# Kernel optimization log

Measured on AMD Instinct MI355X. Metric: run time of the kernel, lower is better.

The kernel has to match this reference:

```python
import jax, jax.numpy as jnp
import numpy as np

N = 50000   # nodes
E = 500000  # edges (before self-loops)
H = 4       # heads
C = 128     # per-head channels
DIN = 182
D1 = H * C  # 512
LN_EPS = 1e-5
NEG_SLOPE = 0.2


def setup_inputs():
    key = jax.random.key(0)
    ks = jax.random.split(key, 26)
    def rn(k, shape, s=0.05):
        return jax.random.normal(k, shape, jnp.float32) * s
    return {
        'x': jax.random.normal(ks[0], (N, DIN), jnp.float32),
        'edge_index': jax.random.randint(ks[1], (2, E), 0, N, jnp.int32),
        # GAT layer 1 (182 -> 4x128)
        'W1': rn(ks[2], (DIN, D1)), 'as1': rn(ks[3], (H, C)), 'ad1': rn(ks[4], (H, C)), 'b1': rn(ks[5], (D1,)),
        # LayerNorm 1
        'g1': jnp.ones((D1,), jnp.float32), 'bn1': jnp.zeros((D1,), jnp.float32),
        # Expansion MLP 512->512->256
        'We1': rn(ks[6], (D1, D1)), 'bE1': rn(ks[7], (D1,)),
        'We2': rn(ks[8], (D1, 256)), 'bE2': rn(ks[9], (256,)),
        # Residual projection 512->256 + learned scale
        'Wr': rn(ks[10], (D1, 256)), 'br': rn(ks[11], (256,)),
        'rscale': jnp.float32(0.5),
        # GAT layer 2 (256 -> 4x128)
        'W2': rn(ks[12], (256, D1)), 'as2': rn(ks[13], (H, C)), 'ad2': rn(ks[14], (H, C)), 'b2': rn(ks[15], (D1,)),
        # LayerNorm 2
        'g2': jnp.ones((D1,), jnp.float32), 'bn2': jnp.zeros((D1,), jnp.float32),
        # Classifier 512->512->2
        'Wc1': rn(ks[16], (D1, D1)), 'bc1': rn(ks[17], (D1,)),
        'Wc2': rn(ks[18], (D1, 2)), 'bc2': rn(ks[19], (2,)),
    }


def layer_norm(x, g, b):
    mu = jnp.mean(x, axis=-1, keepdims=True)
    var = jnp.mean(jnp.square(x - mu), axis=-1, keepdims=True)
    return (x - mu) * jax.lax.rsqrt(var + LN_EPS) * g + b


def gat_conv(x, src, dst, W, a_src, a_dst, bias):
    # PyG GATConv (eval mode, self-loops already in src/dst), concat heads.
    h = (x @ W).reshape(N, H, C)                     # [N,H,C]
    al_s = jnp.sum(h * a_src, axis=-1)               # [N,H]
    al_d = jnp.sum(h * a_dst, axis=-1)               # [N,H]
    e = jax.nn.leaky_relu(al_s[src] + al_d[dst], NEG_SLOPE)  # [E',H]
    m = jax.ops.segment_max(e, dst, num_segments=N)  # segment softmax over target nbhd
    ex = jnp.exp(e - m[dst])
    denom = jax.ops.segment_sum(ex, dst, num_segments=N)
    alpha = ex / denom[dst]                          # [E',H]
    msg = h[src] * alpha[:, :, None]                 # [E',H,C]
    out = jax.ops.segment_sum(msg, dst, num_segments=N)
    return out.reshape(N, H * C) + bias


def reference(x, edge_index, W1, as1, ad1, b1, g1, bn1, We1, bE1, We2, bE2,
              Wr, br, rscale, W2, as2, ad2, b2, g2, bn2, Wc1, bc1, Wc2, bc2):
    loops = jnp.arange(N, dtype=edge_index.dtype)
    src = jnp.concatenate([edge_index[0], loops])    # add self-loops (PyG default)
    dst = jnp.concatenate([edge_index[1], loops])

    h1 = gat_conv(x, src, dst, W1, as1, ad1, b1)
    h1 = jax.nn.elu(layer_norm(h1, g1, bn1))
    h_exp = jax.nn.relu(h1 @ We1 + bE1) @ We2 + bE2  # expansion MLP (dropout=eval)
    h_comb = (h1 @ Wr + br) + rscale * h_exp         # residual combine

    h2 = gat_conv(h_comb, src, dst, W2, as2, ad2, b2)
    h2 = jax.nn.elu(layer_norm(h2, g2, bn2))
    out = jax.nn.relu(h2 @ Wc1 + bc1) @ Wc2 + bc2    # classifier -> [N,2]
    return out
```

## Files before the change

### kernel.cpp

```cpp
#include <hip/hip_runtime.h>
#include <hip/hip_bf16.h>
#include <math.h>

#define NNODES 50000
#define NEDGES 500000
#define NTOT   (NEDGES + NNODES)
#define MPAD   50048
#define D1     512
#define NH     4
#define LN_EPS 1e-5f
#define NEG_SLOPE 0.2f

#define SBLK 256
#define NSB  ((NNODES + SBLK - 1) / SBLK)

typedef __attribute__((ext_vector_type(8))) short short8;
typedef __attribute__((ext_vector_type(4))) float f32x4;
typedef __hip_bfloat16 bf16;

#define GLDS16(g, l) __builtin_amdgcn_global_load_lds( \
    (const __attribute__((address_space(1))) void*)(g), \
    (__attribute__((address_space(3))) void*)(l), 16, 0, 0)

__device__ __forceinline__ float bf2f(short u) {
    unsigned int x = ((unsigned int)(unsigned short)u) << 16;
    return __uint_as_float(x);
}
__device__ __forceinline__ short f2bf(float f) {
    unsigned int x = __float_as_uint(f);
    unsigned int r = (x + 0x7fffu + ((x >> 16) & 1u)) >> 16;
    return (short)r;
}
__device__ __forceinline__ float leaky(float e) {
    return (e >= 0.f) ? e : NEG_SLOPE * e;
}


__global__ void k_count(const int* __restrict__ ei, int* __restrict__ counts) {
    int e = blockIdx.x * blockDim.x + threadIdx.x;
    if (e >= NTOT) return;
    int d = (e < NEDGES) ? ei[NEDGES + e] : (e - NEDGES);
    atomicAdd(&counts[d], 1);
}

__global__ void k_scan1(const int* __restrict__ counts, int* __restrict__ offs,
                        int* __restrict__ bsums) {
    __shared__ int s[SBLK];
    int tid = threadIdx.x, b = blockIdx.x;
    int idx = b * SBLK + tid;
    int v = (idx < NNODES) ? counts[idx] : 0;
    s[tid] = v;
    __syncthreads();
    for (int d = 1; d < SBLK; d <<= 1) {
        int t = (tid >= d) ? s[tid - d] : 0;
        __syncthreads();
        s[tid] += t;
        __syncthreads();
    }
    if (idx < NNODES) offs[idx] = s[tid] - v;
    if (tid == SBLK - 1) bsums[b] = s[tid];
}

__global__ void k_scan2(const int* __restrict__ bsums, int* __restrict__ bbase) {
    __shared__ int s[256];
    int tid = threadIdx.x;
    int v = (tid < NSB) ? bsums[tid] : 0;
    s[tid] = v;
    __syncthreads();
    for (int d = 1; d < 256; d <<= 1) {
        int t = (tid >= d) ? s[tid - d] : 0;
        __syncthreads();
        s[tid] += t;
        __syncthreads();
    }
    bbase[tid] = s[tid] - v;
    if (tid == 255) bbase[256] = s[255];
}

__global__ void k_scan3(int* __restrict__ offs, const int* __restrict__ bbase,
                        int* __restrict__ cursor) {
    int idx = blockIdx.x * 256 + threadIdx.x;
    if (idx < NNODES) {
        int v = offs[idx] + bbase[idx >> 8];
        offs[idx] = v;
        cursor[idx] = v;
    }
    if (idx == 0) offs[NNODES] = bbase[256];
}

__global__ void k_fill(const int* __restrict__ ei, int* __restrict__ cursor,
                       int* __restrict__ srcs) {
    int e = blockIdx.x * blockDim.x + threadIdx.x;
    if (e >= NTOT) return;
    int s, d;
    if (e < NEDGES) { s = ei[e]; d = ei[NEDGES + e]; }
    else            { s = d = e - NEDGES; }
    int pos = atomicAdd(&cursor[d], 1);
    srcs[pos] = s;
}


__global__ void k_wt_all(const float* __restrict__ W1, const float* __restrict__ We1,
                         const float* __restrict__ We2, const float* __restrict__ Wr,
                         const float* __restrict__ W2, const float* __restrict__ Wc1,
                         bf16* __restrict__ W1t, bf16* __restrict__ We1t,
                         bf16* __restrict__ We2t, bf16* __restrict__ Wrt,
                         bf16* __restrict__ W2t, bf16* __restrict__ Wc1t) {
    int which = blockIdx.y;
    const float* W; bf16* Wt; int K, N, Kpad;
    switch (which) {
        case 0:  W = W1;  Wt = W1t;  K = 182; N = 512; Kpad = 192; break;
        case 1:  W = We1; Wt = We1t; K = 512; N = 512; Kpad = 512; break;
        case 2:  W = We2; Wt = We2t; K = 512; N = 256; Kpad = 512; break;
        case 3:  W = Wr;  Wt = Wrt;  K = 512; N = 256; Kpad = 512; break;
        case 4:  W = W2;  Wt = W2t;  K = 256; N = 512; Kpad = 256; break;
        default: W = Wc1; Wt = Wc1t; K = 512; N = 512; Kpad = 512; break;
    }
    int idx = blockIdx.x * 256 + threadIdx.x;
    if (idx >= N * Kpad) return;
    int n = idx / Kpad, k = idx % Kpad;
    float v = (k < K) ? W[(size_t)k * N + n] : 0.f;
    Wt[idx] = __float2bfloat16(v);
}

__global__ void k_xconv(const float* __restrict__ x, bf16* __restrict__ xb) {
    int idx = blockIdx.x * 256 + threadIdx.x;
    if (idx >= MPAD * 192) return;
    int r = idx / 192, k = idx % 192;
    float v = (r < NNODES && k < 182) ? x[(size_t)r * 182 + k] : 0.f;
    xb[idx] = __float2bfloat16(v);
}


__global__ __launch_bounds__(256) void k_edge_alpha(
        const float* __restrict__ als, const float* __restrict__ ald,
        const int* __restrict__ offs, const int* __restrict__ srcs,
        float* __restrict__ alpha) {
    int tid = threadIdx.x;
    int n = blockIdx.x * 4 + (tid >> 6);
    if (n >= NNODES) return;
    int lane = tid & 63;
    int head = lane >> 4, sub = lane & 15;
    int e0 = offs[n], e1 = offs[n + 1];
    float adh = ald[n * NH + head];

    float m = -1e30f;
    for (int k = e0 + sub; k < e1; k += 16)
        m = fmaxf(m, leaky(als[srcs[k] * NH + head] + adh));
    #pragma unroll
    for (int o = 1; o < 16; o <<= 1) m = fmaxf(m, __shfl_xor(m, o));
    float d = 0.f;
    for (int k = e0 + sub; k < e1; k += 16)
        d += __expf(leaky(als[srcs[k] * NH + head] + adh) - m);
    #pragma unroll
    for (int o = 1; o < 16; o <<= 1) d += __shfl_xor(d, o);
    float dinv = 1.f / d;
    for (int k = e0 + sub; k < e1; k += 16)
        alpha[k * NH + head] = __expf(leaky(als[srcs[k] * NH + head] + adh) - m) * dinv;
}


__global__ __launch_bounds__(256) void k_gat_aggregate(
        const bf16* __restrict__ h, const float* __restrict__ alpha,
        const int* __restrict__ offs, const int* __restrict__ srcs,
        const float* __restrict__ bias, const float* __restrict__ gamma,
        const float* __restrict__ beta, bf16* __restrict__ out) {
    int tid = threadIdx.x;
    int n = blockIdx.x * 4 + (tid >> 6);
    if (n >= NNODES) return;
    int lane = tid & 63;
    int head = lane >> 4;
    int ch0 = lane * 8;
    int e0 = offs[n], e1 = offs[n + 1];

    float acc[8] = {};
    for (int base = e0; base < e1; base += 64) {
        int cnt = min(64, e1 - base);
        int sv = (base + lane < e1) ? srcs[base + lane] : 0;
        int k = 0;
        for (; k + 4 <= cnt; k += 4) {
            int s0 = __shfl(sv, k),     s1 = __shfl(sv, k + 1);
            int s2 = __shfl(sv, k + 2), s3 = __shfl(sv, k + 3);
            float p0 = alpha[(base + k)     * NH + head];
            float p1 = alpha[(base + k + 1) * NH + head];
            float p2 = alpha[(base + k + 2) * NH + head];
            float p3 = alpha[(base + k + 3) * NH + head];
            short8 h0 = *reinterpret_cast<const short8*>(&h[(size_t)s0 * D1 + ch0]);
            short8 h1 = *reinterpret_cast<const short8*>(&h[(size_t)s1 * D1 + ch0]);
            short8 h2 = *reinterpret_cast<const short8*>(&h[(size_t)s2 * D1 + ch0]);
            short8 h3 = *reinterpret_cast<const short8*>(&h[(size_t)s3 * D1 + ch0]);
            #pragma unroll
            for (int j = 0; j < 8; j++)
                acc[j] += p0 * bf2f(h0[j]) + p1 * bf2f(h1[j])
                        + p2 * bf2f(h2[j]) + p3 * bf2f(h3[j]);
        }
        for (; k < cnt; k++) {
            int s0 = __shfl(sv, k);
            float p0 = alpha[(base + k) * NH + head];
            short8 h0 = *reinterpret_cast<const short8*>(&h[(size_t)s0 * D1 + ch0]);
            #pragma unroll
            for (int j = 0; j < 8; j++) acc[j] += p0 * bf2f(h0[j]);
        }
    }

    float v[8];
    float ps = 0.f;
    #pragma unroll
    for (int j = 0; j < 8; j++) { v[j] = acc[j] + bias[ch0 + j]; ps += v[j]; }
    #pragma unroll
    for (int o = 1; o < 64; o <<= 1) ps += __shfl_xor(ps, o);
    float mu = ps * (1.f / 512.f);
    float qs = 0.f;
    #pragma unroll
    for (int j = 0; j < 8; j++) { float dvj = v[j] - mu; qs += dvj * dvj; }
    #pragma unroll
    for (int o = 1; o < 64; o <<= 1) qs += __shfl_xor(qs, o);
    float rstd = rsqrtf(qs * (1.f / 512.f) + LN_EPS);

    short8 ov;
    #pragma unroll
    for (int j = 0; j < 8; j++) {
        float y = (v[j] - mu) * rstd * gamma[ch0 + j] + beta[ch0 + j];
        float e = (y > 0.f) ? y : (__expf(y) - 1.f);
        ov[j] = f2bf(e);
    }
    *reinterpret_cast<short8*>(&out[(size_t)n * D1 + ch0]) = ov;
}


#define EPI_BF_LOG   0
#define EPI_BRELU_BF 1
#define EPI_CLS      2

template<int EPI>
__global__ __launch_bounds__(256) void gemm64(
    const ushort* __restrict__ A, const ushort* __restrict__ Bt,
    const float* __restrict__ bias, bf16* __restrict__ Obf,
    float* __restrict__ Of32, const float* __restrict__ Wc2,
    int Mreal, int N, int K, const float* __restrict__ bc2,
    const float* __restrict__ a_s, const float* __restrict__ a_d,
    float* __restrict__ als, float* __restrict__ ald) {
    __shared__ __align__(16) ushort As[128 * 64];
    __shared__ __align__(16) ushort Bs[128 * 64];
    int tid = threadIdx.x;
    int wave = tid >> 6, lane = tid & 63;
    int brow = blockIdx.x * 128;
    int bcol = blockIdx.y * 128;
    int wm = (wave >> 1) * 64, wn = (wave & 1) * 64;
    int lr = lane & 15, hi = lane >> 4;
    int rx = lr & 7;
    int r8 = lane >> 3;
    int slotsw = (lane & 7) ^ r8;

    f32x4 acc[4][4] = {};

    for (int k0 = 0; k0 < K; k0 += 64) {
        if (k0) __syncthreads();
        #pragma unroll
        for (int i = 0; i < 4; i++) {
            int rb = wave * 32 + i * 8;
            GLDS16(A  + (size_t)(brow + rb + r8) * K + k0 + slotsw * 8, As + rb * 64);
            GLDS16(Bt + (size_t)(bcol + rb + r8) * K + k0 + slotsw * 8, Bs + rb * 64);
        }
        __syncthreads();

        #pragma unroll
        for (int sub = 0; sub < 2; sub++) {
            short8 af[4], bfr[4];
            int bsl = ((sub * 4 + hi) ^ rx) * 8;
            #pragma unroll
            for (int f = 0; f < 4; f++) {
                af[f]  = *reinterpret_cast<const short8*>(&As[(wm + f * 16 + lr) * 64 + bsl]);
                bfr[f] = *reinterpret_cast<const short8*>(&Bs[(wn + f * 16 + lr) * 64 + bsl]);
            }
            #pragma unroll
            for (int fm = 0; fm < 4; fm++)
                #pragma unroll
                for (int fn = 0; fn < 4; fn++)
                    acc[fm][fn] = __builtin_amdgcn_mfma_f32_16x16x32_bf16(
                        af[fm], bfr[fn], acc[fm][fn], 0, 0, 0);
        }
    }

    if (EPI == EPI_BF_LOG) {
        int head = bcol >> 7;
        float asr[4], adr[4];
        #pragma unroll
        for (int fn = 0; fn < 4; fn++) {
            int col = bcol + wn + fn * 16 + lr;
            asr[fn] = a_s[col]; adr[fn] = a_d[col];
        }
        #pragma unroll
        for (int fm = 0; fm < 4; fm++) {
            int row0 = brow + wm + fm * 16 + hi * 4;
            #pragma unroll
            for (int r = 0; r < 4; r++) {
                int row = row0 + r;
                bool ok = row < Mreal;
                float s1 = 0.f, s2 = 0.f;
                #pragma unroll
                for (int fn = 0; fn < 4; fn++) {
                    float v = acc[fm][fn][r];
                    if (ok) Obf[(size_t)row * N + bcol + wn + fn * 16 + lr] = __float2bfloat16(v);
                    s1 += v * asr[fn];
                    s2 += v * adr[fn];
                }
                #pragma unroll
                for (int o = 1; o < 16; o <<= 1) {
                    s1 += __shfl_xor(s1, o);
                    s2 += __shfl_xor(s2, o);
                }
                if (ok && lr == 0) {
                    atomicAdd(&als[row * NH + head], s1);
                    atomicAdd(&ald[row * NH + head], s2);
                }
            }
        }
        return;
    }

    if (EPI == EPI_CLS) {
        float w2[4][2], b4[4];
        #pragma unroll
        for (int fn = 0; fn < 4; fn++) {
            int col = bcol + wn + fn * 16 + lr;
            w2[fn][0] = Wc2[col * 2];
            w2[fn][1] = Wc2[col * 2 + 1];
            b4[fn] = bias[col];
        }
        #pragma unroll
        for (int fm = 0; fm < 4; fm++) {
            #pragma unroll
            for (int r = 0; r < 4; r++) {
                int row = brow + wm + fm * 16 + hi * 4 + r;
                float s0 = 0.f, s1 = 0.f;
                #pragma unroll
                for (int fn = 0; fn < 4; fn++) {
                    float v = acc[fm][fn][r] + b4[fn];
                    v = v > 0.f ? v : 0.f;
                    s0 += v * w2[fn][0];
                    s1 += v * w2[fn][1];
                }
                #pragma unroll
                for (int o = 1; o < 16; o <<= 1) {
                    s0 += __shfl_xor(s0, o);
                    s1 += __shfl_xor(s1, o);
                }
                if (lr == 0 && row < Mreal) {
                    if (bcol == 0 && wn == 0) { s0 += bc2[0]; s1 += bc2[1]; }
                    atomicAdd(&Of32[row * 2],     s0);
                    atomicAdd(&Of32[row * 2 + 1], s1);
                }
            }
        }
        return;
    }

    #pragma unroll
    for (int fm = 0; fm < 4; fm++) {
        int row0 = brow + wm + fm * 16 + hi * 4;
        #pragma unroll
        for (int fn = 0; fn < 4; fn++) {
            int col = bcol + wn + fn * 16 + lr;
            #pragma unroll
            for (int r = 0; r < 4; r++) {
                int row = row0 + r;
                if (row >= Mreal) continue;
                float v = acc[fm][fn][r] + bias[col];
                v = v > 0.f ? v : 0.f;
                Obf[(size_t)row * N + col] = __float2bfloat16(v);
            }
        }
    }
}


__global__ __launch_bounds__(256) void gemm_dual64(
    const ushort* __restrict__ A1, const ushort* __restrict__ B1t,
    const ushort* __restrict__ A2, const ushort* __restrict__ B2t,
    const float* __restrict__ bias1, const float* __restrict__ bias2,
    bf16* __restrict__ Obf, int Mreal, int N, int K,
    const float* __restrict__ rsc) {
    __shared__ __align__(16) ushort As[128 * 64];
    __shared__ __align__(16) ushort Bs[128 * 64];
    int tid = threadIdx.x;
    int wave = tid >> 6, lane = tid & 63;
    int brow = blockIdx.x * 128;
    int bcol = blockIdx.y * 128;
    int wm = (wave >> 1) * 64, wn = (wave & 1) * 64;
    int lr = lane & 15, hi = lane >> 4;
    int rx = lr & 7;
    int r8 = lane >> 3;
    int slotsw = (lane & 7) ^ r8;
    float rs = *rsc;

    f32x4 acc[4][4] = {};

    #pragma unroll
    for (int phase = 0; phase < 2; phase++) {
        const ushort* Ap = phase ? A2 : A1;
        const ushort* Bp = phase ? B2t : B1t;
        if (phase) {
            __syncthreads();
            #pragma unroll
            for (int fm = 0; fm < 4; fm++)
                #pragma unroll
                for (int fn = 0; fn < 4; fn++)
                    #pragma unroll
                    for (int r = 0; r < 4; r++) acc[fm][fn][r] *= rs;
        }
        for (int k0 = 0; k0 < K; k0 += 64) {
            if (k0 || phase) __syncthreads();
            #pragma unroll
            for (int i = 0; i < 4; i++) {
                int rb = wave * 32 + i * 8;
                GLDS16(Ap + (size_t)(brow + rb + r8) * K + k0 + slotsw * 8, As + rb * 64);
                GLDS16(Bp + (size_t)(bcol + rb + r8) * K + k0 + slotsw * 8, Bs + rb * 64);
            }
            __syncthreads();

            #pragma unroll
            for (int sub = 0; sub < 2; sub++) {
                short8 af[4], bfr[4];
                int bsl = ((sub * 4 + hi) ^ rx) * 8;
                #pragma unroll
                for (int f = 0; f < 4; f++) {
                    af[f]  = *reinterpret_cast<const short8*>(&As[(wm + f * 16 + lr) * 64 + bsl]);
                    bfr[f] = *reinterpret_cast<const short8*>(&Bs[(wn + f * 16 + lr) * 64 + bsl]);
                }
                #pragma unroll
                for (int fm = 0; fm < 4; fm++)
                    #pragma unroll
                    for (int fn = 0; fn < 4; fn++)
                        acc[fm][fn] = __builtin_amdgcn_mfma_f32_16x16x32_bf16(
                            af[fm], bfr[fn], acc[fm][fn], 0, 0, 0);
            }
        }
    }

    #pragma unroll
    for (int fm = 0; fm < 4; fm++) {
        int row0 = brow + wm + fm * 16 + hi * 4;
        #pragma unroll
        for (int fn = 0; fn < 4; fn++) {
            int col = bcol + wn + fn * 16 + lr;
            float be = bias2[col] + rs * bias1[col];
            #pragma unroll
            for (int r = 0; r < 4; r++) {
                int row = row0 + r;
                if (row >= Mreal) continue;
                Obf[(size_t)row * N + col] = __float2bfloat16(acc[fm][fn][r] + be);
            }
        }
    }
}


extern "C" void kernel_launch(void* const* d_in, const int* in_sizes, int n_in,
                              void* d_out, int out_size, void* d_ws, size_t ws_size,
                              hipStream_t stream) {
    const float* x   = (const float*)d_in[0];
    const int*   ei  = (const int*)d_in[1];
    const float* W1  = (const float*)d_in[2];
    const float* as1 = (const float*)d_in[3];
    const float* ad1 = (const float*)d_in[4];
    const float* b1  = (const float*)d_in[5];
    const float* g1  = (const float*)d_in[6];
    const float* bn1 = (const float*)d_in[7];
    const float* We1 = (const float*)d_in[8];
    const float* bE1 = (const float*)d_in[9];
    const float* We2 = (const float*)d_in[10];
    const float* bE2 = (const float*)d_in[11];
    const float* Wr  = (const float*)d_in[12];
    const float* br  = (const float*)d_in[13];
    const float* rsc = (const float*)d_in[14];
    const float* W2  = (const float*)d_in[15];
    const float* as2 = (const float*)d_in[16];
    const float* ad2 = (const float*)d_in[17];
    const float* b2  = (const float*)d_in[18];
    const float* g2  = (const float*)d_in[19];
    const float* bn2 = (const float*)d_in[20];
    const float* Wc1 = (const float*)d_in[21];
    const float* bc1 = (const float*)d_in[22];
    const float* Wc2 = (const float*)d_in[23];
    const float* bc2 = (const float*)d_in[24];
    float* out = (float*)d_out;

    char* ws = (char*)d_ws;
    size_t o = 0;
    auto alloc = [&](size_t bytes) { void* p = ws + o; o += (bytes + 255) & ~255ull; return p; };
    bf16* xb    = (bf16*)alloc((size_t)MPAD * 192 * 2);
    bf16* bufA  = (bf16*)alloc((size_t)MPAD * D1 * 2);
    bf16* bufB  = (bf16*)alloc((size_t)MPAD * D1 * 2);
    bf16* bufC  = (bf16*)alloc((size_t)MPAD * D1 * 2);
    bf16* hcb   = (bf16*)alloc((size_t)MPAD * 256 * 2);
    bf16* W1t   = (bf16*)alloc((size_t)512 * 192 * 2);
    bf16* We1t  = (bf16*)alloc((size_t)512 * 512 * 2);
    bf16* We2t  = (bf16*)alloc((size_t)256 * 512 * 2);
    bf16* Wrt   = (bf16*)alloc((size_t)256 * 512 * 2);
    bf16* W2t   = (bf16*)alloc((size_t)512 * 256 * 2);
    bf16* Wc1t  = (bf16*)alloc((size_t)512 * 512 * 2);
    float* als  = (float*)alloc((size_t)NNODES * NH * 4);
    float* ald  = (float*)alloc((size_t)NNODES * NH * 4);
    float* alpha= (float*)alloc((size_t)NTOT * NH * 4);
    int* counts = (int*)alloc((NNODES + 1) * 4);
    int* offs   = (int*)alloc((NNODES + 1) * 4);
    int* cursor = (int*)alloc((NNODES + 1) * 4);
    int* srcs   = (int*)alloc((size_t)NTOT * 4);
    int* bsums  = (int*)alloc((NSB + 1) * 4);
    int* bbase  = (int*)alloc(257 * 4);

    hipMemsetAsync(counts, 0, NNODES * 4, stream);
    k_count<<<(NTOT + 255) / 256, 256, 0, stream>>>(ei, counts);
    k_scan1<<<NSB, SBLK, 0, stream>>>(counts, offs, bsums);
    k_scan2<<<1, 256, 0, stream>>>(bsums, bbase);
    k_scan3<<<(NNODES + 255) / 256, 256, 0, stream>>>(offs, bbase, cursor);
    k_fill<<<(NTOT + 255) / 256, 256, 0, stream>>>(ei, cursor, srcs);

    k_wt_all<<<dim3(1024, 6), 256, 0, stream>>>(W1, We1, We2, Wr, W2, Wc1,
                                                W1t, We1t, We2t, Wrt, W2t, Wc1t);
    k_xconv<<<(MPAD * 192 + 255) / 256, 256, 0, stream>>>(x, xb);

    dim3 blk(256);
    dim3 g512(MPAD / 128, 4), g256(MPAD / 128, 2);
    int nwb = (NNODES + 3) / 4;

    hipMemsetAsync(als, 0, (size_t)NNODES * NH * 4 * 2, stream);
    gemm64<EPI_BF_LOG><<<g512, blk, 0, stream>>>((const ushort*)xb, (const ushort*)W1t,
        nullptr, bufA, nullptr, nullptr, NNODES, 512, 192, nullptr, as1, ad1, als, ald);
    k_edge_alpha<<<nwb, blk, 0, stream>>>(als, ald, offs, srcs, alpha);
    k_gat_aggregate<<<nwb, blk, 0, stream>>>(bufA, alpha, offs, srcs, b1, g1, bn1, bufB);

    gemm64<EPI_BRELU_BF><<<g512, blk, 0, stream>>>((const ushort*)bufB, (const ushort*)We1t,
        bE1, bufC, nullptr, nullptr, NNODES, 512, 512, nullptr, nullptr, nullptr, nullptr, nullptr);
    gemm_dual64<<<g256, blk, 0, stream>>>((const ushort*)bufC, (const ushort*)We2t,
        (const ushort*)bufB, (const ushort*)Wrt, bE2, br, hcb, NNODES, 256, 512, rsc);

    hipMemsetAsync(als, 0, (size_t)NNODES * NH * 4 * 2, stream);
    gemm64<EPI_BF_LOG><<<g512, blk, 0, stream>>>((const ushort*)hcb, (const ushort*)W2t,
        nullptr, bufA, nullptr, nullptr, NNODES, 512, 256, nullptr, as2, ad2, als, ald);
    k_edge_alpha<<<nwb, blk, 0, stream>>>(als, ald, offs, srcs, alpha);
    k_gat_aggregate<<<nwb, blk, 0, stream>>>(bufA, alpha, offs, srcs, b2, g2, bn2, bufB);

    hipMemsetAsync(out, 0, (size_t)out_size * 4, stream);
    gemm64<EPI_CLS><<<g512, blk, 0, stream>>>((const ushort*)bufB, (const ushort*)Wc1t,
        bc1, nullptr, out, Wc2, NNODES, 512, 512, bc2, nullptr, nullptr, nullptr, nullptr);
}
```

Baseline: 585.2 us.

## Compute attention logits via precomputed W·a vectors instead of GEMM epilogue atomics

Folds the attention vectors into the projection weights (W·a_src, W·a_dst), giving small K×8 matrices. A separate kernel computes per-node logits straight from the bf16 input rows, and the GEMM epilogue no longer does shuffle reductions and atomicAdds. This removes atomic traffic, the memsets and epilogue register pressure. In exchange it adds an extra pass over the input activations, and each logits thread reads its row with scalar, uncoalesced loads. Logits now come from bf16 inputs with fp32 folded weights rather than from the fp32 accumulator.

```diff
diff --git a/kernel.cpp b/kernel.cpp
--- a/kernel.cpp
+++ b/kernel.cpp
@@ -129,6 +129,48 @@
     int r = idx / 192, k = idx % 192;
     float v = (r < NNODES && k < 182) ? x[(size_t)r * 182 + k] : 0.f;
     xb[idx] = __float2bfloat16(v);
+}
+
+
+__global__ void k_wsd(const float* __restrict__ W1, const float* __restrict__ as1,
+                      const float* __restrict__ ad1, const float* __restrict__ W2,
+                      const float* __restrict__ as2, const float* __restrict__ ad2,
+                      float* __restrict__ wsd1, float* __restrict__ wsd2) {
+    int idx = blockIdx.x * 256 + threadIdx.x;
+    if (idx < 192 * 8) {
+        int k = idx >> 3, j = idx & 7;
+        int hh = j & 3;
+        float s = 0.f;
+        if (k < 182) {
+            const float* a = (j < 4) ? as1 : ad1;
+            for (int c = 0; c < 128; c++)
+                s += W1[(size_t)k * 512 + hh * 128 + c] * a[hh * 128 + c];
+        }
+        wsd1[idx] = s;
+    } else if (idx < 192 * 8 + 256 * 8) {
+        int i2 = idx - 192 * 8;
+        int k = i2 >> 3, j = i2 & 7;
+        int hh = j & 3;
+        const float* a = (j < 4) ? as2 : ad2;
+        float s = 0.f;
+        for (int c = 0; c < 128; c++)
+            s += W2[(size_t)k * 512 + hh * 128 + c] * a[hh * 128 + c];
+        wsd2[i2] = s;
+    }
+}
+
+
+__global__ void k_logits(const bf16* __restrict__ A, const float* __restrict__ wsd,
+                         float* __restrict__ als, float* __restrict__ ald, int K) {
+    int idx = blockIdx.x * 256 + threadIdx.x;
+    if (idx >= NNODES * 8) return;
+    int n = idx >> 3, j = idx & 7;
+    const short* row = (const short*)(A + (size_t)n * K);
+    float s = 0.f;
+    #pragma unroll 4
+    for (int k = 0; k < K; k++) s += bf2f(row[k]) * wsd[k * 8 + j];
+    if (j < 4) als[n * NH + j] = s;
+    else       ald[n * NH + (j - 4)] = s;
 }
 
 
@@ -228,7 +270,7 @@
 }
 
 
-#define EPI_BF_LOG   0
+#define EPI_BF       0
 #define EPI_BRELU_BF 1
 #define EPI_CLS      2
 
@@ -237,9 +279,7 @@
     const ushort* __restrict__ A, const ushort* __restrict__ Bt,
     const float* __restrict__ bias, bf16* __restrict__ Obf,
     float* __restrict__ Of32, const float* __restrict__ Wc2,
-    int Mreal, int N, int K, const float* __restrict__ bc2,
-    const float* __restrict__ a_s, const float* __restrict__ a_d,
-    float* __restrict__ als, float* __restrict__ ald) {
+    int Mreal, int N, int K, const float* __restrict__ bc2) {
     __shared__ __align__(16) ushort As[128 * 64];
     __shared__ __align__(16) ushort Bs[128 * 64];
     int tid = threadIdx.x;
@@ -280,43 +320,6 @@
                     acc[fm][fn] = __builtin_amdgcn_mfma_f32_16x16x32_bf16(
                         af[fm], bfr[fn], acc[fm][fn], 0, 0, 0);
         }
-    }
-
-    if (EPI == EPI_BF_LOG) {
-        int head = bcol >> 7;
-        float asr[4], adr[4];
-        #pragma unroll
-        for (int fn = 0; fn < 4; fn++) {
-            int col = bcol + wn + fn * 16 + lr;
-            asr[fn] = a_s[col]; adr[fn] = a_d[col];
-        }
-        #pragma unroll
-        for (int fm = 0; fm < 4; fm++) {
-            int row0 = brow + wm + fm * 16 + hi * 4;
-            #pragma unroll
-            for (int r = 0; r < 4; r++) {
-                int row = row0 + r;
-                bool ok = row < Mreal;
-                float s1 = 0.f, s2 = 0.f;
-                #pragma unroll
-                for (int fn = 0; fn < 4; fn++) {
-                    float v = acc[fm][fn][r];
-                    if (ok) Obf[(size_t)row * N + bcol + wn + fn * 16 + lr] = __float2bfloat16(v);
-                    s1 += v * asr[fn];
-                    s2 += v * adr[fn];
-                }
-                #pragma unroll
-                for (int o = 1; o < 16; o <<= 1) {
-                    s1 += __shfl_xor(s1, o);
-                    s2 += __shfl_xor(s2, o);
-                }
-                if (ok && lr == 0) {
-                    atomicAdd(&als[row * NH + head], s1);
-                    atomicAdd(&ald[row * NH + head], s2);
-                }
-            }
-        }
-        return;
     }
 
     if (EPI == EPI_CLS) {
@@ -366,8 +369,8 @@
             for (int r = 0; r < 4; r++) {
                 int row = row0 + r;
                 if (row >= Mreal) continue;
-                float v = acc[fm][fn][r] + bias[col];
-                v = v > 0.f ? v : 0.f;
+                float v = acc[fm][fn][r];
+                if (EPI == EPI_BRELU_BF) { v += bias[col]; v = v > 0.f ? v : 0.f; }
                 Obf[(size_t)row * N + col] = __float2bfloat16(v);
             }
         }
@@ -500,6 +503,8 @@
     bf16* Wrt   = (bf16*)alloc((size_t)256 * 512 * 2);
     bf16* W2t   = (bf16*)alloc((size_t)512 * 256 * 2);
     bf16* Wc1t  = (bf16*)alloc((size_t)512 * 512 * 2);
+    float* wsd1 = (float*)alloc(192 * 8 * 4);
+    float* wsd2 = (float*)alloc(256 * 8 * 4);
     float* als  = (float*)alloc((size_t)NNODES * NH * 4);
     float* ald  = (float*)alloc((size_t)NNODES * NH * 4);
     float* alpha= (float*)alloc((size_t)NTOT * NH * 4);
@@ -520,29 +525,31 @@
     k_wt_all<<<dim3(1024, 6), 256, 0, stream>>>(W1, We1, We2, Wr, W2, Wc1,
                                                 W1t, We1t, We2t, Wrt, W2t, Wc1t);
     k_xconv<<<(MPAD * 192 + 255) / 256, 256, 0, stream>>>(x, xb);
+    k_wsd<<<14, 256, 0, stream>>>(W1, as1, ad1, W2, as2, ad2, wsd1, wsd2);
 
     dim3 blk(256);
     dim3 g512(MPAD / 128, 4), g256(MPAD / 128, 2);
     int nwb = (NNODES + 3) / 4;
-
-    hipMemsetAsync(als, 0, (size_t)NNODES * NH * 4 * 2, stream);
-    gemm64<EPI_BF_LOG><<<g512, blk, 0, stream>>>((const ushort*)xb, (const ushort*)W1t,
-        nullptr, bufA, nullptr, nullptr, NNODES, 512, 192, nullptr, as1, ad1, als, ald);
+    int nlb = (NNODES * 8 + 255) / 256;
+
+    k_logits<<<nlb, blk, 0, stream>>>(xb, wsd1, als, ald, 192);
+    gemm64<EPI_BF><<<g512, blk, 0, stream>>>((const ushort*)xb, (const ushort*)W1t,
+        nullptr, bufA, nullptr, nullptr, NNODES, 512, 192, nullptr);
     k_edge_alpha<<<nwb, blk, 0, stream>>>(als, ald, offs, srcs, alpha);
     k_gat_aggregate<<<nwb, blk, 0, stream>>>(bufA, alpha, offs, srcs, b1, g1, bn1, bufB);
 
     gemm64<EPI_BRELU_BF><<<g512, blk, 0, stream>>>((const ushort*)bufB, (const ushort*)We1t,
-        bE1, bufC, nullptr, nullptr, NNODES, 512, 512, nullptr, nullptr, nullptr, nullptr, nullptr);
+        bE1, bufC, nullptr, nullptr, NNODES, 512, 512, nullptr);
     gemm_dual64<<<g256, blk, 0, stream>>>((const ushort*)bufC, (const ushort*)We2t,
         (const ushort*)bufB, (const ushort*)Wrt, bE2, br, hcb, NNODES, 256, 512, rsc);
 
-    hipMemsetAsync(als, 0, (size_t)NNODES * NH * 4 * 2, stream);
-    gemm64<EPI_BF_LOG><<<g512, blk, 0, stream>>>((const ushort*)hcb, (const ushort*)W2t,
-        nullptr, bufA, nullptr, nullptr, NNODES, 512, 256, nullptr, as2, ad2, als, ald);
+    k_logits<<<nlb, blk, 0, stream>>>(hcb, wsd2, als, ald, 256);
+    gemm64<EPI_BF><<<g512, blk, 0, stream>>>((const ushort*)hcb, (const ushort*)W2t,
+        nullptr, bufA, nullptr, nullptr, NNODES, 512, 256, nullptr);
     k_edge_alpha<<<nwb, blk, 0, stream>>>(als, ald, offs, srcs, alpha);
     k_gat_aggregate<<<nwb, blk, 0, stream>>>(bufA, alpha, offs, srcs, b2, g2, bn2, bufB);
 
     hipMemsetAsync(out, 0, (size_t)out_size * 4, stream);
     gemm64<EPI_CLS><<<g512, blk, 0, stream>>>((const ushort*)bufB, (const ushort*)Wc1t,
-        bc1, nullptr, out, Wc2, NNODES, 512, 512, bc2, nullptr, nullptr, nullptr, nullptr);
-}
+        bc1, nullptr, out, Wc2, NNODES, 512, 512, bc2);
+}
```

Result: no change. 578.6 us (-1.1%).
